# Performance work log

Hardware: AMD Instinct MI355X
Metric: run time of the kernel (lower is better)

The kernel has to match this reference:

```python
import jax, jax.numpy as jnp
import numpy as np

# tf.image.rgb_to_grayscale luma weights; grayscale->rgb duplicates channels, so the
# rgb->gray after an identical per-channel gather reduces to scaling by sum(weights).
RGB_WSUM = np.float32(0.2989 + 0.5870 + 0.1140)


def _inverse_logpolar_indices(H, W):
    """Nearest-neighbor gather indices mapping a log-polar image (theta rows,
    rho cols) back to Cartesian coordinates (inverse log-polar remap)."""
    cy, cx = (H - 1) / 2.0, (W - 1) / 2.0
    ys, xs = np.meshgrid(np.arange(H, dtype=np.float64),
                         np.arange(W, dtype=np.float64), indexing='ij')
    dy, dx = ys - cy, xs - cx
    r = np.sqrt(dx * dx + dy * dy)
    rmax = np.sqrt(cx * cx + cy * cy)
    rho = np.where(r > 0.5, np.log(np.maximum(r, 1e-6)) / np.log(rmax) * (W - 1), 0.0)
    theta = (np.arctan2(dy, dx) + np.pi) / (2.0 * np.pi) * (H - 1)
    rho_i = np.clip(np.rint(rho), 0, W - 1).astype(np.int32)
    th_i = np.clip(np.rint(theta), 0, H - 1).astype(np.int32)
    return jnp.asarray(th_i), jnp.asarray(rho_i)  # each (H, W)


def setup_inputs() -> dict:
    key = jax.random.key(0)
    B, H, W, C = 1, 256, 256, 512
    inputs = jax.random.normal(key, (B, H, W, C), dtype=jnp.float32)
    return {"inputs": inputs}


def reference(inputs) -> jnp.ndarray:
    B, H, W, C = inputs.shape  # H == W required by the original layer's transpose/reshape
    # tf.transpose(tf.squeeze(inputs,0)) reverses all dims: (H,W,C) -> (C,W,H);
    # each channel is then tf.reshape'd to (H,W) (identity in memory for H==W).
    x = jnp.transpose(inputs[0], (2, 1, 0))  # (C, W, H) == (C, H, W) layout for square
    th_i, rho_i = _inverse_logpolar_indices(H, W)
    # Vectorized over channels: identical gather for every channel (replaces tf.map_fn).
    warped = x[:, th_i, rho_i]  # (C, H, W) irregular gather
    out = warped * RGB_WSUM      # gray->rgb (tile) -> warp -> rgb->gray collapses to a scale
    # tf.reshape((C,H,W) -> self.shape=(1,H,W,C)) is a raw row-major reshape (faithful).
    return jnp.reshape(out, (1, H, W, C))
```

## Files before the change

### kernel.cpp

```cpp
#include <hip/hip_runtime.h>
#include <math.h>


typedef float v4f __attribute__((ext_vector_type(4)));

__global__ __launch_bounds__(256) void InverseLogPolar_kernel(
        const float* __restrict__ in, float* __restrict__ out) {
    __shared__ int   sBase[256];
    __shared__ float tile[32 * 260];

    const int b    = blockIdx.x;
    const int row  = ((b & 7) << 5) | ((b >> 3) & 31);
    const int ct   = b >> 8;
    const int t    = threadIdx.x;
    const int pix0 = row << 8;
    const int c0   = ct << 5;

    {
        const int i = row;
        const int j = t;
        const double dy = (double)i - 127.5;
        const double dx = (double)j - 127.5;
        const double r  = sqrt(dx * dx + dy * dy);
        const double rmax  = sqrt(127.5 * 127.5 + 127.5 * 127.5);
        const double lrmax = log(rmax);
        double rho   = (r > 0.5) ? (log(fmax(r, 1e-6)) / lrmax) * 255.0 : 0.0;
        double theta = ((atan2(dy, dx) + M_PI) / (2.0 * M_PI)) * 255.0;
        double rr = fmin(fmax(rint(rho),   0.0), 255.0);
        double tt = fmin(fmax(rint(theta), 0.0), 255.0);
        sBase[t] = ((int)rr << 17) | ((int)tt << 9);
    }
    __syncthreads();

    const float WSUM = (float)(0.2989 + 0.587 + 0.114);

    float4 v[8];
    #pragma unroll
    for (int it = 0; it < 8; ++it) {
        const int k = (it << 8) + t;
        const int p = k >> 3;
        const int cj = (k & 7) << 2;
        v[it] = *reinterpret_cast<const float4*>(in + sBase[p] + c0 + cj);
    }
    #pragma unroll
    for (int it = 0; it < 8; ++it) {
        const int k = (it << 8) + t;
        const int p = k >> 3;
        const int cj = (k & 7) << 2;
        tile[(cj + 0) * 260 + p] = v[it].x * WSUM;
        tile[(cj + 1) * 260 + p] = v[it].y * WSUM;
        tile[(cj + 2) * 260 + p] = v[it].z * WSUM;
        tile[(cj + 3) * 260 + p] = v[it].w * WSUM;
    }
    __syncthreads();

    const int l = t & 63;
    const int w = t >> 6;
    #pragma unroll
    for (int it2 = 0; it2 < 8; ++it2) {
        const int c = (w << 3) + it2;
        const v4f o = *reinterpret_cast<const v4f*>(&tile[c * 260 + (l << 2)]);
        __builtin_nontemporal_store(
            o, reinterpret_cast<v4f*>(out + ((size_t)(c0 + c) << 16) + pix0 + (l << 2)));
    }
}

extern "C" void kernel_launch(void* const* d_in, const int* in_sizes, int n_in,
                              void* d_out, int out_size, void* d_ws, size_t ws_size,
                              hipStream_t stream) {
    const float* in = (const float*)d_in[0];
    float* out = (float*)d_out;
    dim3 grid(4096);
    dim3 block(256);
    hipLaunchKernelGGL(InverseLogPolar_kernel, grid, block, 0, stream, in, out);
}
```

Measured before the change: 32.93 us.

## Process two output rows per block with XOR-swizzled shared tile

Each block now handles two output rows (512 pixels) for 32 channels, halving the grid and doubling the gather loads per thread. The padded transpose tile is replaced by an unpadded 512-wide tile with an XOR swizzle on pixel index to avoid LDS bank conflicts. The aim is more memory-level parallelism and longer contiguous stores. In exchange, shared memory per block roughly doubles and register use rises, which may reduce occupancy.

```diff
diff --git a/kernel.cpp b/kernel.cpp
--- a/kernel.cpp
+++ b/kernel.cpp
@@ -6,18 +6,19 @@
 
 __global__ __launch_bounds__(256) void InverseLogPolar_kernel(
         const float* __restrict__ in, float* __restrict__ out) {
-    __shared__ int   sBase[256];
-    __shared__ float tile[32 * 260];
+    __shared__ int   sBase[512];
+    __shared__ float tile[32 * 512];
 
     const int b    = blockIdx.x;
-    const int row  = ((b & 7) << 5) | ((b >> 3) & 31);
-    const int ct   = b >> 8;
+    const int rp   = ((b & 7) << 4) | ((b >> 3) & 15);
+    const int ct   = b >> 7;
     const int t    = threadIdx.x;
-    const int pix0 = row << 8;
+    const int pix0 = rp << 9;
     const int c0   = ct << 5;
 
-    {
-        const int i = row;
+    #pragma unroll
+    for (int h = 0; h < 2; ++h) {
+        const int i = (rp << 1) + h;
         const int j = t;
         const double dy = (double)i - 127.5;
         const double dx = (double)j - 127.5;
@@ -28,40 +29,46 @@
         double theta = ((atan2(dy, dx) + M_PI) / (2.0 * M_PI)) * 255.0;
         double rr = fmin(fmax(rint(rho),   0.0), 255.0);
         double tt = fmin(fmax(rint(theta), 0.0), 255.0);
-        sBase[t] = ((int)rr << 17) | ((int)tt << 9);
+        sBase[(h << 8) + t] = ((int)rr << 17) | ((int)tt << 9);
     }
     __syncthreads();
 
     const float WSUM = (float)(0.2989 + 0.587 + 0.114);
 
-    float4 v[8];
+    float4 v[16];
     #pragma unroll
-    for (int it = 0; it < 8; ++it) {
+    for (int it = 0; it < 16; ++it) {
         const int k = (it << 8) + t;
         const int p = k >> 3;
         const int cj = (k & 7) << 2;
         v[it] = *reinterpret_cast<const float4*>(in + sBase[p] + c0 + cj);
     }
     #pragma unroll
-    for (int it = 0; it < 8; ++it) {
+    for (int it = 0; it < 16; ++it) {
         const int k = (it << 8) + t;
         const int p = k >> 3;
         const int cj = (k & 7) << 2;
-        tile[(cj + 0) * 260 + p] = v[it].x * WSUM;
-        tile[(cj + 1) * 260 + p] = v[it].y * WSUM;
-        tile[(cj + 2) * 260 + p] = v[it].z * WSUM;
-        tile[(cj + 3) * 260 + p] = v[it].w * WSUM;
+        const int pp = p ^ ((k & 7) << 2);
+        float* r0 = &tile[cj * 512 + pp];
+        r0[0]    = v[it].x * WSUM;
+        r0[512]  = v[it].y * WSUM;
+        r0[1024] = v[it].z * WSUM;
+        r0[1536] = v[it].w * WSUM;
     }
     __syncthreads();
 
     const int l = t & 63;
     const int w = t >> 6;
     #pragma unroll
-    for (int it2 = 0; it2 < 8; ++it2) {
-        const int c = (w << 3) + it2;
-        const v4f o = *reinterpret_cast<const v4f*>(&tile[c * 260 + (l << 2)]);
+    for (int it2 = 0; it2 < 16; ++it2) {
+        const int c    = (w << 3) + (it2 >> 1);
+        const int half = it2 & 1;
+        const int s    = ((c >> 2) & 7) << 2;
+        const v4f o = *reinterpret_cast<const v4f*>(
+            &tile[c * 512 + (half << 8) + ((l << 2) ^ s)]);
         __builtin_nontemporal_store(
-            o, reinterpret_cast<v4f*>(out + ((size_t)(c0 + c) << 16) + pix0 + (l << 2)));
+            o, reinterpret_cast<v4f*>(out + ((size_t)(c0 + c) << 16) + pix0
+                                          + (half << 8) + (l << 2)));
     }
 }
 
@@ -70,7 +77,7 @@
                               hipStream_t stream) {
     const float* in = (const float*)d_in[0];
     float* out = (float*)d_out;
-    dim3 grid(4096);
+    dim3 grid(2048);
     dim3 block(256);
     hipLaunchKernelGGL(InverseLogPolar_kernel, grid, block, 0, stream, in, out);
 }
```

Measured after the change: 33.24 us. No clear change (+1.0%).
